# Kernel optimization log

Hardware: AMD Instinct MI355X
Metric: run time of the kernel (lower is better)

Reference implementation:

```python
import jax, jax.numpy as jnp
import numpy as np

# video grid and attention geometry (must match init_kwargs)
F_T, H_T, W_T = 4, 32, 32
K = 3                      # kernel_size (odd)
P = K // 2
T = F_T * H_T * W_T        # max_num_tokens = 4096
HEADS = 8
DIM_HEAD = 64
SCALE = DIM_HEAD ** -0.5
DIM = 512
INNER = HEADS * DIM_HEAD


def _build_window_indices():
    # flat token index grid, padded with sentinel T (out-of-range -> zero row after gather)
    idx = np.arange(T).reshape(F_T, H_T, W_T)
    padded = np.full((F_T + 2 * P, H_T + 2 * P, W_T + 2 * P), T, dtype=np.int64)
    padded[P:P + F_T, P:P + H_T, P:P + W_T] = idx
    # [T, K^3] neighborhood indices, kernel offsets in (kf, kh, kw) C-order (matches unfoldNd)
    win = np.lib.stride_tricks.sliding_window_view(padded, (K, K, K)).reshape(T, K ** 3)
    # causal: mask keys whose flat index is strictly in the future of the query
    causal = np.arange(T)[:, None] < win
    causal = np.concatenate([np.zeros((T, 1), dtype=bool), causal], axis=1)  # BOS column never masked
    return jnp.asarray(win), jnp.asarray(causal)

WIN_IDX, CAUSAL_MASK = _build_window_indices()


def setup_inputs() -> dict:
    key = jax.random.key(0)
    k0, k1, k2, k3 = jax.random.split(key, 4)
    n = T  # 1 BOS + (T-1) video tokens; padding logic pads body to exactly T tokens
    x = jax.random.normal(k0, (2, n, DIM), dtype=jnp.float32)
    Wq = jax.random.normal(k1, (DIM, INNER), dtype=jnp.float32) * (DIM ** -0.5)
    Wkv = jax.random.normal(k2, (DIM, 2 * INNER), dtype=jnp.float32) * (DIM ** -0.5)
    Wo = jax.random.normal(k3, (INNER, DIM), dtype=jnp.float32) * (INNER ** -0.5)
    bo = jnp.zeros((DIM,), dtype=jnp.float32)
    return {"x": x, "Wq": Wq, "Wkv": Wkv, "Wo": Wo, "bo": bo}


def _split_heads(t, b):
    # [b, n, h*d] -> [(b*h), n, d]
    n = t.shape[1]
    return t.reshape(b, n, HEADS, DIM_HEAD).transpose(0, 2, 1, 3).reshape(b * HEADS, n, DIM_HEAD)


def reference(x, Wq, Wkv, Wo, bo):
    b, n, _ = x.shape
    tpf = H_T * W_T
    padding = tpf - (n - 1) % tpf  # pads body tokens to a multiple of tokens_per_frame
    x = jnp.pad(x, ((0, 0), (0, padding), (0, 0)))
    q = x @ Wq
    k, v = jnp.split(x @ Wkv, 2, axis=-1)
    q, k, v = (_split_heads(t, b) for t in (q, k, v))
    bh = b * HEADS
    q = q[:, 1:] * SCALE            # drop BOS query; [bh, T, d]
    bos_v = v[:, :1]                # BOS attends only to itself -> its value passes through
    k_bos, k = k[:, :1], k[:, 1:]
    v_bos, v = v[:, :1], v[:, 1:]
    # gather K^3 3D neighborhoods; sentinel index T maps to a zero row
    zero_row = jnp.zeros((bh, 1, DIM_HEAD), dtype=k.dtype)
    k_nb = jnp.concatenate([k, zero_row], axis=1)[:, WIN_IDX]   # [bh, T, K^3, d]
    v_nb = jnp.concatenate([v, zero_row], axis=1)[:, WIN_IDX]
    # prepend global BOS key/value to every window
    k_nb = jnp.concatenate([jnp.broadcast_to(k_bos[:, :, None], (bh, T, 1, DIM_HEAD)), k_nb], axis=2)
    v_nb = jnp.concatenate([jnp.broadcast_to(v_bos[:, :, None], (bh, T, 1, DIM_HEAD)), v_nb], axis=2)
    sim = jnp.einsum('bid,bijd->bij', q, k_nb)                  # [bh, T, K^3+1]
    sim = jnp.where(CAUSAL_MASK[None], -jnp.finfo(sim.dtype).max, sim)
    attn = jax.nn.softmax(sim, axis=-1)
    out = jnp.einsum('bij,bijd->bid', attn, v_nb)               # [bh, T, d]
    out = jnp.concatenate([bos_v, out], axis=1)                 # [bh, T+1, d]
    np_tok = out.shape[1]
    out = out.reshape(b, HEADS, np_tok, DIM_HEAD).transpose(0, 2, 1, 3).reshape(b, np_tok, INNER)
    return (out @ Wo + bo)[:, :n]
```

## Files before the change

kernel.cpp:

```cpp
#include <hip/hip_runtime.h>


#define T_TOK   4096
#define DIM     512
#define NQKV    1536

typedef unsigned short u16;
typedef unsigned int   u32;
typedef unsigned long long u64;
typedef __attribute__((ext_vector_type(8))) short short8;
typedef __attribute__((ext_vector_type(4))) float f32x4;

__device__ __forceinline__ u16 f2bf(float f) {
    u32 u = __float_as_uint(f);
    return (u16)((u + 0x7fffu + ((u >> 16) & 1u)) >> 16);
}
__device__ __forceinline__ float b2f(u16 u) {
    return __uint_as_float(((u32)u) << 16);
}

__device__ __forceinline__ void gload_lds16(const void* g, void* l) {
    __builtin_amdgcn_global_load_lds(
        (const __attribute__((address_space(1))) void*)g,
        (__attribute__((address_space(3))) void*)l, 16, 0, 0);
}

__global__ void cast_all_kernel(const float4* __restrict__ x,
                                const float* __restrict__ Wq, const float* __restrict__ Wkv,
                                const float* __restrict__ Wo,
                                u16* __restrict__ xb, u16* __restrict__ Wt,
                                u16* __restrict__ Wot) {
    __shared__ float S[64 * 65];
    int blk = blockIdx.x;
    int tid = threadIdx.x;
    if (blk < 4096) {
        int i = blk * 256 + tid;
        float4 v = x[i];
        u64 pack = (u64)f2bf(v.x) | ((u64)f2bf(v.y) << 16) |
                   ((u64)f2bf(v.z) << 32) | ((u64)f2bf(v.w) << 48);
        ((u64*)xb)[i] = pack;
        return;
    }
    int isWo = blk >= 4288;
    int tIdx = isWo ? (blk - 4288) : (blk - 4096);
    int tn = tIdx >> 3, tk = tIdx & 7;
    #pragma unroll
    for (int p = 0; p < 16; ++p) {
        int kl = p * 4 + (tid >> 6), nl = tid & 63;
        int gk = tk * 64 + kl, gn = tn * 64 + nl;
        float v;
        if (isWo)            v = Wo[gk * 512 + gn];
        else if (gn < 512)   v = Wq[gk * 512 + gn];
        else                 v = Wkv[gk * 1024 + (gn - 512)];
        S[kl * 65 + nl] = v;
    }
    __syncthreads();
    u16* dst = isWo ? Wot : Wt;
    #pragma unroll
    for (int p = 0; p < 16; ++p) {
        int nl = p * 4 + (tid >> 6), kl = tid & 63;
        dst[(size_t)(tn * 64 + nl) * 512 + tk * 64 + kl] = f2bf(S[kl * 65 + nl]);
    }
}

template <int BM, int BN, int MODE>
__global__ __launch_bounds__(256)
void gemm_nt(const u16* __restrict__ A, const u16* __restrict__ B,
             void* __restrict__ Cv, const float* __restrict__ bias,
             int lda, int ldb, int ldc) {
    constexpr int K = 512, BK = 32, KSTEPS = K / BK;
    constexpr int ACH = BM * 4;
    constexpr int NCH = (BM + BN) * 4;
    constexpr int NLD = NCH / 256;
    constexpr int ABYTES = BM * 64;
    constexpr int HALF = (BM + BN) * 64;
    constexpr int MI = BM / 32, NJ = BN / 32;
    __shared__ __align__(16) char lds[2 * HALF];
    const int tid  = threadIdx.x;
    const int lane = tid & 63, wave = tid >> 6;
    const int quad = lane >> 4, mrow = lane & 15;
    const int wm = wave >> 1, wn = wave & 1;

    const int nblk = gridDim.x * gridDim.y;
    int lid = blockIdx.y * gridDim.x + blockIdx.x;
    if (!(nblk & 7)) lid = (lid & 7) * (nblk >> 3) + (lid >> 3);
    const int bm = lid / (int)gridDim.x, bn = lid % (int)gridDim.x;

    const char* gptr[NLD];
    char*       lptr[NLD];
    #pragma unroll
    for (int it = 0; it < NLD; ++it) {
        int c   = it * 256 + tid;
        int inB = (c >= ACH);
        int a   = inB ? c - ACH : c;
        int r   = a >> 2;
        int kc  = ((a & 3) - (r >> 1)) & 3;
        int row = (inB ? bn * BN : bm * BM) + r;
        const u16* base = inB ? B : A;
        int ld = inB ? ldb : lda;
        gptr[it] = (const char*)(base + (size_t)row * ld + kc * 8);
        lptr[it] = (char*)lds + (it * 256 + wave * 64) * 16;
    }
    const char* aLds[MI];
    const char* bLds[NJ];
    #pragma unroll
    for (int i = 0; i < MI; ++i) {
        int ra = wm * (BM / 2) + i * 16 + mrow;
        aLds[i] = lds + (ra * 4 + ((quad + (ra >> 1)) & 3)) * 16;
    }
    #pragma unroll
    for (int j = 0; j < NJ; ++j) {
        int rb = wn * (BN / 2) + j * 16 + mrow;
        bLds[j] = lds + ABYTES + (rb * 4 + ((quad + (rb >> 1)) & 3)) * 16;
    }

    f32x4 acc[MI][NJ] = {};
    #pragma unroll
    for (int it = 0; it < NLD; ++it)
        gload_lds16(gptr[it], lptr[it]);

    #pragma unroll
    for (int ks = 0; ks < KSTEPS; ++ks) {
        const int cur = ks & 1;
        if (ks + 1 < KSTEPS) {
            #pragma unroll
            for (int it = 0; it < NLD; ++it)
                gload_lds16(gptr[it] + 2 * (ks + 1) * BK, lptr[it] + (cur ^ 1) * HALF);
            asm volatile("s_waitcnt vmcnt(%0)" :: "i"(NLD) : "memory");
        } else {
            asm volatile("s_waitcnt vmcnt(0)" ::: "memory");
        }
        asm volatile("s_barrier" ::: "memory");

        short8 af[MI], bf[NJ];
        #pragma unroll
        for (int i = 0; i < MI; ++i) af[i] = *(const short8*)(aLds[i] + cur * HALF);
        #pragma unroll
        for (int j = 0; j < NJ; ++j) bf[j] = *(const short8*)(bLds[j] + cur * HALF);
        #pragma unroll
        for (int i = 0; i < MI; ++i)
            #pragma unroll
            for (int j = 0; j < NJ; ++j)
                acc[i][j] = __builtin_amdgcn_mfma_f32_16x16x32_bf16(af[i], bf[j], acc[i][j], 0, 0, 0);
        asm volatile("s_waitcnt lgkmcnt(0)" ::: "memory");
        asm volatile("s_barrier" ::: "memory");
    }

    #pragma unroll
    for (int i = 0; i < MI; ++i) {
        #pragma unroll
        for (int j = 0; j < NJ; ++j) {
            int colg = bn * BN + wn * (BN / 2) + j * 16 + mrow;
            #pragma unroll
            for (int r = 0; r < 4; ++r) {
                int rowg = bm * BM + wm * (BM / 2) + i * 16 + quad * 4 + r;
                if (MODE == 0) {
                    ((u16*)Cv)[(size_t)rowg * ldc + colg] = f2bf(acc[i][j][r]);
                } else {
                    ((float*)Cv)[(size_t)rowg * ldc + colg] = acc[i][j][r] + bias[colg];
                }
            }
        }
    }
}

__global__ __launch_bounds__(256)
void attn_kernel(const u16* __restrict__ QKV, u16* __restrict__ O) {
    __shared__ float Pns[4][64];
    const int wave = threadIdx.x >> 6;
    const int bsw = ((blockIdx.x & 7) << 9) | (blockIdx.x >> 3);
    const int wid  = bsw * 4 + wave;
    const int lane = threadIdx.x & 63;
    const int b  = wid >> 13;
    const int hp = (wid >> 12) & 1;
    const int ti = wid & 4095;
    const size_t baseQ = (size_t)b * T_TOK * NQKV;
    const size_t baseO = (size_t)b * T_TOK * DIM;
    const int hbase = hp * 256;

    if (ti == 0) {
        #pragma unroll
        for (int hd = 0; hd < 4; ++hd)
            O[baseO + hbase + hd * 64 + lane] =
                QKV[baseQ + 1024 + hbase + hd * 64 + lane];
        return;
    }
    const int t = ti - 1;
    const int f = t >> 10, hh = (t >> 5) & 31, ww = t & 31;

    const int j = lane >> 2, g = lane & 3;
    int jm1 = j - 1;
    int dh9 = ((jm1 * 11) >> 5) - 1;
    int dw9 = jm1 - (dh9 + 1) * 3 - 1;
    int df = (j >= 1 && j <= 9) ? -1 : 0;
    int dh = (j >= 1 && j <= 9) ? dh9 : ((j >= 10 && j <= 12) ? -1 : 0);
    int dw = (j >= 1 && j <= 9) ? dw9 :
             ((j >= 10 && j <= 12) ? (j - 11) : ((j == 13) ? -1 : 0));
    int nf = f + df, nh = hh + dh, nw = ww + dw;
    int valid = (nf >= 0) && ((unsigned)nh < 32u) && ((unsigned)nw < 32u)
                && (j >= 1) && (j <= 14);
    int p = valid ? (t + 1 + df * 1024 + dh * 32 + dw) : 0;
    int score_on = valid || (j == 0);

    const u16* qbase = QKV + baseQ + (size_t)(t + 1) * NQKV + hbase + g * 16;
    const u16* kbase = QKV + baseQ + (size_t)p * NQKV + 512 + hbase + g * 16;
    short8 qa[4], qb[4], ka[4], kb[4];
    #pragma unroll
    for (int hd = 0; hd < 4; ++hd) {
        qa[hd] = *(const short8*)(qbase + hd * 64);
        qb[hd] = *(const short8*)(qbase + hd * 64 + 8);
        ka[hd] = *(const short8*)(kbase + hd * 64);
        kb[hd] = *(const short8*)(kbase + hd * 64 + 8);
    }
    float s[4] = {};
    #pragma unroll
    for (int i = 0; i < 8; ++i)
        #pragma unroll
        for (int hd = 0; hd < 4; ++hd) {
            s[hd] = fmaf(b2f((u16)qa[hd][i]), b2f((u16)ka[hd][i]), s[hd]);
            s[hd] = fmaf(b2f((u16)qb[hd][i]), b2f((u16)kb[hd][i]), s[hd]);
        }
    #pragma unroll
    for (int hd = 0; hd < 4; ++hd) {
        s[hd] += __shfl_xor(s[hd], 1);
        s[hd] += __shfl_xor(s[hd], 2);
        s[hd] *= 0.125f;
        s[hd] = score_on ? s[hd] : -3.0e38f;
    }
    float m[4] = {s[0], s[1], s[2], s[3]};
    #pragma unroll
    for (int off = 4; off <= 32; off <<= 1)
        #pragma unroll
        for (int hd = 0; hd < 4; ++hd)
            m[hd] = fmaxf(m[hd], __shfl_xor(m[hd], off));
    float pe[4], l[4];
    #pragma unroll
    for (int hd = 0; hd < 4; ++hd) {
        pe[hd] = __expf(s[hd] - m[hd]);
        l[hd] = pe[hd];
    }
    #pragma unroll
    for (int off = 4; off <= 32; off <<= 1)
        #pragma unroll
        for (int hd = 0; hd < 4; ++hd)
            l[hd] += __shfl_xor(l[hd], off);
    u32 voff = (u32)p * 3072u;

    if ((lane & 3) == 0) {
        int slot = lane >> 2;
        #pragma unroll
        for (int hd = 0; hd < 4; ++hd)
            Pns[wave][hd * 16 + slot] = pe[hd] * __frcp_rn(l[hd]);
    }
    asm volatile("s_waitcnt lgkmcnt(0)" ::: "memory");

    const float* ptab = &Pns[wave][(lane >> 4) * 16];
    const char* vrow = (const char*)(QKV + baseQ + 1024 + hbase) + lane * 8;
    float a0 = 0.f, a1 = 0.f, a2 = 0.f, a3 = 0.f;
    #pragma unroll
    for (int jj = 0; jj < 15; ++jj) {
        u32 o = (u32)__builtin_amdgcn_readlane((int)voff, jj * 4);
        float pj = ptab[jj];
        u64 v = *(const u64*)(vrow + o);
        u32 lo = (u32)v, hi = (u32)(v >> 32);
        a0 = fmaf(pj, __uint_as_float(lo << 16), a0);
        a1 = fmaf(pj, __uint_as_float(lo & 0xffff0000u), a1);
        a2 = fmaf(pj, __uint_as_float(hi << 16), a2);
        a3 = fmaf(pj, __uint_as_float(hi & 0xffff0000u), a3);
    }
    u64 pack = (u64)f2bf(a0) | ((u64)f2bf(a1) << 16) |
               ((u64)f2bf(a2) << 32) | ((u64)f2bf(a3) << 48);
    *(u64*)((char*)(O + baseO + (size_t)ti * DIM + hbase) + lane * 8) = pack;
}

extern "C" void kernel_launch(void* const* d_in, const int* in_sizes, int n_in,
                              void* d_out, int out_size, void* d_ws, size_t ws_size,
                              hipStream_t stream) {
    const float* x   = (const float*)d_in[0];
    const float* Wq  = (const float*)d_in[1];
    const float* Wkv = (const float*)d_in[2];
    const float* Wo  = (const float*)d_in[3];
    const float* bo  = (const float*)d_in[4];
    float* out = (float*)d_out;
    char* ws = (char*)d_ws;

    u16* xb  = (u16*)(ws + 0);
    u16* Wt  = (u16*)(ws + 8388608);
    u16* Wot = (u16*)(ws + 9961472);
    u16* QKV = (u16*)(ws + 10485760);
    u16* O   = (u16*)(ws + 0);

    cast_all_kernel<<<dim3(4352), dim3(256), 0, stream>>>(
        (const float4*)x, Wq, Wkv, Wo, xb, Wt, Wot);
    gemm_nt<128, 128, 0><<<dim3(12, 64), dim3(256), 0, stream>>>(
        xb, Wt, (void*)QKV, nullptr, 512, 512, 1536);
    attn_kernel<<<dim3(4096), dim3(256), 0, stream>>>(QKV, O);
    gemm_nt<128, 64, 1><<<dim3(8, 64), dim3(256), 0, stream>>>(
        O, Wot, (void*)out, bo, 512, 512, 512);
}
```

Measured before the change: 132.2 us.

## Process all heads per wave and compute window scores with MFMA

The attention kernel now assigns one token with all eight heads to each wave instead of a head pair. Query-key scores are computed with bf16 MFMA instructions by replicating the query row across lanes, and only one output element per lane is used. The PV accumulation uses 16-byte loads and packed FMAs. This halves the grid and cuts scalar FMA and shuffle work, at the cost of wasted MFMA lanes and more registers per wave.

```diff
diff --git a/kernel.cpp b/kernel.cpp
--- a/kernel.cpp
+++ b/kernel.cpp
@@ -10,6 +10,7 @@
 typedef unsigned long long u64;
 typedef __attribute__((ext_vector_type(8))) short short8;
 typedef __attribute__((ext_vector_type(4))) float f32x4;
+typedef __attribute__((ext_vector_type(2))) float f32x2;
 
 __device__ __forceinline__ u16 f2bf(float f) {
     u32 u = __float_as_uint(f);
@@ -166,29 +167,26 @@
 
 __global__ __launch_bounds__(256)
 void attn_kernel(const u16* __restrict__ QKV, u16* __restrict__ O) {
-    __shared__ float Pns[4][64];
+    __shared__ float Pns[4][8 * 17];
     const int wave = threadIdx.x >> 6;
-    const int bsw = ((blockIdx.x & 7) << 9) | (blockIdx.x >> 3);
+    const int bsw = ((blockIdx.x & 7) << 8) | (blockIdx.x >> 3);
     const int wid  = bsw * 4 + wave;
     const int lane = threadIdx.x & 63;
-    const int b  = wid >> 13;
-    const int hp = (wid >> 12) & 1;
+    const int b  = wid >> 12;
     const int ti = wid & 4095;
     const size_t baseQ = (size_t)b * T_TOK * NQKV;
     const size_t baseO = (size_t)b * T_TOK * DIM;
-    const int hbase = hp * 256;
 
     if (ti == 0) {
-        #pragma unroll
-        for (int hd = 0; hd < 4; ++hd)
-            O[baseO + hbase + hd * 64 + lane] =
-                QKV[baseQ + 1024 + hbase + hd * 64 + lane];
+        const uint4* src = (const uint4*)(QKV + baseQ + 1024);
+        uint4* dst = (uint4*)(O + baseO);
+        dst[lane] = src[lane];
         return;
     }
     const int t = ti - 1;
     const int f = t >> 10, hh = (t >> 5) & 31, ww = t & 31;
 
-    const int j = lane >> 2, g = lane & 3;
+    const int j = lane & 15, quad = lane >> 4;
     int jm1 = j - 1;
     int dh9 = ((jm1 * 11) >> 5) - 1;
     int dw9 = jm1 - (dh9 + 1) * 3 - 1;
@@ -202,75 +200,70 @@
     int p = valid ? (t + 1 + df * 1024 + dh * 32 + dw) : 0;
     int score_on = valid || (j == 0);
 
-    const u16* qbase = QKV + baseQ + (size_t)(t + 1) * NQKV + hbase + g * 16;
-    const u16* kbase = QKV + baseQ + (size_t)p * NQKV + 512 + hbase + g * 16;
-    short8 qa[4], qb[4], ka[4], kb[4];
-    #pragma unroll
-    for (int hd = 0; hd < 4; ++hd) {
-        qa[hd] = *(const short8*)(qbase + hd * 64);
-        qb[hd] = *(const short8*)(qbase + hd * 64 + 8);
-        ka[hd] = *(const short8*)(kbase + hd * 64);
-        kb[hd] = *(const short8*)(kbase + hd * 64 + 8);
-    }
-    float s[4] = {};
-    #pragma unroll
-    for (int i = 0; i < 8; ++i)
-        #pragma unroll
-        for (int hd = 0; hd < 4; ++hd) {
-            s[hd] = fmaf(b2f((u16)qa[hd][i]), b2f((u16)ka[hd][i]), s[hd]);
-            s[hd] = fmaf(b2f((u16)qb[hd][i]), b2f((u16)kb[hd][i]), s[hd]);
-        }
-    #pragma unroll
-    for (int hd = 0; hd < 4; ++hd) {
-        s[hd] += __shfl_xor(s[hd], 1);
-        s[hd] += __shfl_xor(s[hd], 2);
-        s[hd] *= 0.125f;
-        s[hd] = score_on ? s[hd] : -3.0e38f;
-    }
-    float m[4] = {s[0], s[1], s[2], s[3]};
-    #pragma unroll
-    for (int off = 4; off <= 32; off <<= 1)
-        #pragma unroll
-        for (int hd = 0; hd < 4; ++hd)
-            m[hd] = fmaxf(m[hd], __shfl_xor(m[hd], off));
-    float pe[4], l[4];
-    #pragma unroll
-    for (int hd = 0; hd < 4; ++hd) {
-        pe[hd] = __expf(s[hd] - m[hd]);
-        l[hd] = pe[hd];
-    }
-    #pragma unroll
-    for (int off = 4; off <= 32; off <<= 1)
-        #pragma unroll
-        for (int hd = 0; hd < 4; ++hd)
-            l[hd] += __shfl_xor(l[hd], off);
+    const u16* qrow = QKV + baseQ + (size_t)(t + 1) * NQKV;
+    const u16* krow = QKV + baseQ + (size_t)p * NQKV + 512;
+    const f32x4 zero = {0.f, 0.f, 0.f, 0.f};
+    float s[8];
+    #pragma unroll
+    for (int h = 0; h < 8; ++h) {
+        short8 qa = *(const short8*)(qrow + h * 64 + quad * 8);
+        short8 ka = *(const short8*)(krow + h * 64 + quad * 8);
+        short8 qb = *(const short8*)(qrow + h * 64 + 32 + quad * 8);
+        short8 kb = *(const short8*)(krow + h * 64 + 32 + quad * 8);
+        f32x4 acc = __builtin_amdgcn_mfma_f32_16x16x32_bf16(qa, ka, zero, 0, 0, 0);
+        acc = __builtin_amdgcn_mfma_f32_16x16x32_bf16(qb, kb, acc, 0, 0, 0);
+        s[h] = acc[0] * 0.125f;
+    }
+    #pragma unroll
+    for (int h = 0; h < 8; ++h) s[h] = score_on ? s[h] : -3.0e38f;
+
+    float m[8], pe[8], l[8];
+    #pragma unroll
+    for (int h = 0; h < 8; ++h) m[h] = s[h];
+    #pragma unroll
+    for (int off = 1; off <= 8; off <<= 1)
+        #pragma unroll
+        for (int h = 0; h < 8; ++h) m[h] = fmaxf(m[h], __shfl_xor(m[h], off));
+    #pragma unroll
+    for (int h = 0; h < 8; ++h) { pe[h] = __expf(s[h] - m[h]); l[h] = pe[h]; }
+    #pragma unroll
+    for (int off = 1; off <= 8; off <<= 1)
+        #pragma unroll
+        for (int h = 0; h < 8; ++h) l[h] += __shfl_xor(l[h], off);
+
     u32 voff = (u32)p * 3072u;
 
-    if ((lane & 3) == 0) {
-        int slot = lane >> 2;
-        #pragma unroll
-        for (int hd = 0; hd < 4; ++hd)
-            Pns[wave][hd * 16 + slot] = pe[hd] * __frcp_rn(l[hd]);
+    if (lane < 16) {
+        #pragma unroll
+        for (int h = 0; h < 8; ++h)
+            Pns[wave][h * 17 + lane] = pe[h] * __frcp_rn(l[h]);
     }
     asm volatile("s_waitcnt lgkmcnt(0)" ::: "memory");
 
-    const float* ptab = &Pns[wave][(lane >> 4) * 16];
-    const char* vrow = (const char*)(QKV + baseQ + 1024 + hbase) + lane * 8;
-    float a0 = 0.f, a1 = 0.f, a2 = 0.f, a3 = 0.f;
+    const float* ptab = &Pns[wave][(lane >> 3) * 17];
+    const char* vbase = (const char*)(QKV + baseQ + 1024) + lane * 16;
+    f32x2 a01 = {0.f, 0.f}, a23 = {0.f, 0.f}, a45 = {0.f, 0.f}, a67 = {0.f, 0.f};
     #pragma unroll
     for (int jj = 0; jj < 15; ++jj) {
-        u32 o = (u32)__builtin_amdgcn_readlane((int)voff, jj * 4);
+        u32 o = (u32)__builtin_amdgcn_readlane((int)voff, jj);
         float pj = ptab[jj];
-        u64 v = *(const u64*)(vrow + o);
-        u32 lo = (u32)v, hi = (u32)(v >> 32);
-        a0 = fmaf(pj, __uint_as_float(lo << 16), a0);
-        a1 = fmaf(pj, __uint_as_float(lo & 0xffff0000u), a1);
-        a2 = fmaf(pj, __uint_as_float(hi << 16), a2);
-        a3 = fmaf(pj, __uint_as_float(hi & 0xffff0000u), a3);
-    }
-    u64 pack = (u64)f2bf(a0) | ((u64)f2bf(a1) << 16) |
-               ((u64)f2bf(a2) << 32) | ((u64)f2bf(a3) << 48);
-    *(u64*)((char*)(O + baseO + (size_t)ti * DIM + hbase) + lane * 8) = pack;
+        uint4 v = *(const uint4*)(vbase + o);
+        f32x2 p2 = {pj, pj};
+        f32x2 v0 = {__uint_as_float(v.x << 16), __uint_as_float(v.x & 0xffff0000u)};
+        f32x2 v1 = {__uint_as_float(v.y << 16), __uint_as_float(v.y & 0xffff0000u)};
+        f32x2 v2 = {__uint_as_float(v.z << 16), __uint_as_float(v.z & 0xffff0000u)};
+        f32x2 v3 = {__uint_as_float(v.w << 16), __uint_as_float(v.w & 0xffff0000u)};
+        a01 = __builtin_elementwise_fma(p2, v0, a01);
+        a23 = __builtin_elementwise_fma(p2, v1, a23);
+        a45 = __builtin_elementwise_fma(p2, v2, a45);
+        a67 = __builtin_elementwise_fma(p2, v3, a67);
+    }
+    u32 r0 = (u32)f2bf(a01.x) | ((u32)f2bf(a01.y) << 16);
+    u32 r1 = (u32)f2bf(a23.x) | ((u32)f2bf(a23.y) << 16);
+    u32 r2 = (u32)f2bf(a45.x) | ((u32)f2bf(a45.y) << 16);
+    u32 r3 = (u32)f2bf(a67.x) | ((u32)f2bf(a67.y) << 16);
+    uint4 pack = {r0, r1, r2, r3};
+    *(uint4*)((char*)(O + baseO) + (size_t)ti * (DIM * 2) + lane * 16) = pack;
 }
 
 extern "C" void kernel_launch(void* const* d_in, const int* in_sizes, int n_in,
@@ -294,7 +287,7 @@
         (const float4*)x, Wq, Wkv, Wo, xb, Wt, Wot);
     gemm_nt<128, 128, 0><<<dim3(12, 64), dim3(256), 0, stream>>>(
         xb, Wt, (void*)QKV, nullptr, 512, 512, 1536);
-    attn_kernel<<<dim3(4096), dim3(256), 0, stream>>>(QKV, O);
+    attn_kernel<<<dim3(2048), dim3(256), 0, stream>>>(QKV, O);
     gemm_nt<128, 64, 1><<<dim3(8, 64), dim3(256), 0, stream>>>(
         O, Wot, (void*)out, bo, 512, 512, 512);
 }
```

Measured after the change: 138.5 us. +4.8%, slower.
